# Performance work log

Hardware: AMD Instinct MI355X
Metric: run time of the kernel (lower is better)

## Reference

```python
import jax, jax.numpy as jnp
import numpy as np

N = 50000
E = 500000
H = 128


def _linear(x, w, b):
    # torch nn.Linear: y = x @ W.T + b, W is [out, in]
    return x @ w.T + b


def _layer(x, h, edge_index, w0_w, w0_b, wl_w, wl_b, w1_w, w1_b):
    # PyG MessagePassing(aggr='add', flow='target_to_source'):
    # x_j = h[edge_index[1]], scatter-add into edge_index[0], dim_size = N
    msg = h[edge_index[1]]                               # [E, H] gather
    aggr = jax.ops.segment_sum(msg, edge_index[0], num_segments=h.shape[0])  # [N, H]
    return _linear(aggr, wl_w, wl_b) + _linear(h, w0_w, w0_b) + _linear(x, w1_w, w1_b)


def setup_inputs() -> dict:
    key = jax.random.key(0)
    ks = jax.random.split(key, 12)
    wscale = 0.05
    return {
        "x_a": jax.random.normal(ks[0], (N, H), jnp.float32),
        "x_b": jax.random.normal(ks[1], (N, H), jnp.float32),
        "edge_ab": jax.random.randint(ks[2], (2, E), 0, N, jnp.int32),
        "edge_ba": jax.random.randint(ks[3], (2, E), 0, N, jnp.int32),
        "conv0_w0_w": jax.random.normal(ks[4], (H, H), jnp.float32) * wscale,
        "conv0_w0_b": jnp.zeros((H,), jnp.float32),
        "conv0_wl_w": jax.random.normal(ks[5], (H, H), jnp.float32) * wscale,
        "conv0_wl_b": jnp.zeros((H,), jnp.float32),
        "conv0_w1_w": jax.random.normal(ks[6], (H, H), jnp.float32) * wscale,
        "conv0_w1_b": jnp.zeros((H,), jnp.float32),
        "conv1_w0_w": jax.random.normal(ks[7], (H, H), jnp.float32) * wscale,
        "conv1_w0_b": jnp.zeros((H,), jnp.float32),
        "conv1_wl_w": jax.random.normal(ks[8], (H, H), jnp.float32) * wscale,
        "conv1_wl_b": jnp.zeros((H,), jnp.float32),
        "conv1_w1_w": jax.random.normal(ks[9], (H, H), jnp.float32) * wscale,
        "conv1_w1_b": jnp.zeros((H,), jnp.float32),
        "out_w": jax.random.normal(ks[10], (H, H), jnp.float32) * wscale,
        "out_b": jnp.zeros((H,), jnp.float32),
    }


def reference(x_a, x_b, edge_ab, edge_ba,
              conv0_w0_w, conv0_w0_b, conv0_wl_w, conv0_wl_b, conv0_w1_w, conv0_w1_b,
              conv1_w0_w, conv1_w0_b, conv1_wl_w, conv1_wl_b, conv1_w1_w, conv1_w1_b,
              out_w, out_b):
    # metapath = [(a, r1, b), (b, r2, a)], loop over reversed(metapath):
    # iter 0: conv_idx=1, edge (b, r2, a), dst='a'
    h_a = jax.nn.relu(_layer(x_a, x_a, edge_ba,
                             conv1_w0_w, conv1_w0_b, conv1_wl_w, conv1_wl_b, conv1_w1_w, conv1_w1_b))
    # iter 1: conv_idx=0, edge (a, r1, b), dst='b'
    h_b = jax.nn.relu(_layer(x_b, x_b, edge_ab,
                             conv0_w0_w, conv0_w0_b, conv0_wl_w, conv0_wl_b, conv0_w1_w, conv0_w1_b))
    # start_type = 'a'
    return _linear(h_a, out_w, out_b)
```

## Files before the change

kernel.cpp:

```cpp
#include <hip/hip_runtime.h>
#include <hip/hip_bf16.h>

#define NN 50000
#define NE 500000
#define HD 128
#define CAP 128
#define PREP_B 24
#define ZCUR_B ((NN + 255) / 256)
#define ZAGGR_B 6250
#define FILLB_B ((NE + 255) / 256)
#define XCONV_B 3125
#define K2_B (FILLB_B + XCONV_B)

typedef __bf16 bf16;
typedef __attribute__((ext_vector_type(8))) __bf16 bf16x8;
typedef __attribute__((ext_vector_type(4))) float floatx4;

__device__ inline float u2f(unsigned int lo16) {
    union { unsigned int i; float f; } c; c.i = lo16 << 16; return c.f;
}

__device__ inline bf16x8 cvt8(floatx4 a, floatx4 b) {
    bf16x8 r;
#pragma unroll
    for (int j = 0; j < 4; j++) { r[j] = (bf16)a[j]; r[j + 4] = (bf16)b[j]; }
    return r;
}

__device__ inline void split8(const floatx4 f0, const floatx4 f1, bf16x8& hi, bf16x8& lo) {
#pragma unroll
    for (int j = 0; j < 4; j++) {
        float a = f0[j]; bf16 h = (bf16)a; hi[j] = h; lo[j] = (bf16)(a - (float)h);
        float b = f1[j]; bf16 g = (bf16)b; hi[j + 4] = g; lo[j + 4] = (bf16)(b - (float)g);
    }
}

__device__ inline bf16x8 zero8() {
    bf16x8 v;
#pragma unroll
    for (int j = 0; j < 8; j++) v[j] = (bf16)0.f;
    return v;
}

__device__ inline void addrow(floatx4& f0, floatx4& f1, const uint4 v) {
    f0[0] += u2f(v.x & 0xffff); f0[1] += u2f(v.x >> 16);
    f0[2] += u2f(v.y & 0xffff); f0[3] += u2f(v.y >> 16);
    f1[0] += u2f(v.z & 0xffff); f1[1] += u2f(v.z >> 16);
    f1[2] += u2f(v.w & 0xffff); f1[3] += u2f(v.w >> 16);
}

__global__ __launch_bounds__(256) void k_setup1(
    const float* __restrict__ wl, const float* __restrict__ w0, const float* __restrict__ w1,
    const float* __restrict__ bl, const float* __restrict__ b0, const float* __restrict__ b1,
    const float* __restrict__ ow, const float* __restrict__ ob,
    bf16* __restrict__ wlb, bf16* __restrict__ w01b, bf16* __restrict__ owb,
    float* __restrict__ bias1, float* __restrict__ bias2,
    float* __restrict__ aggr, int* __restrict__ cur, int* __restrict__ ovf_cnt, int tier)
{
    const int b = blockIdx.x, tid = threadIdx.x;
    if (b < PREP_B) {
        int g = b * 256 + tid;
        int m = g >> 11, off = (g & 2047) << 3;
        if (m == 0) {
            const floatx4 a = *(const floatx4*)(wl + off);
            const floatx4 c = *(const floatx4*)(wl + off + 4);
            *(bf16x8*)(wlb + off) = cvt8(a, c);
        } else if (m == 1) {
            floatx4 a = *(const floatx4*)(w0 + off);
            floatx4 c = *(const floatx4*)(w0 + off + 4);
            const floatx4 d = *(const floatx4*)(w1 + off);
            const floatx4 e = *(const floatx4*)(w1 + off + 4);
#pragma unroll
            for (int j = 0; j < 4; j++) { a[j] += d[j]; c[j] += e[j]; }
            *(bf16x8*)(w01b + off) = cvt8(a, c);
        } else {
            const floatx4 a = *(const floatx4*)(ow + off);
            const floatx4 c = *(const floatx4*)(ow + off + 4);
            *(bf16x8*)(owb + off) = cvt8(a, c);
        }
        if (g < 128) bias1[g] = bl[g] + b0[g] + b1[g];
        else if (g < 256) bias2[g - 128] = ob[g - 128];
    } else if (b < PREP_B + ZCUR_B) {
        if (tier >= 1) {
            int i = (b - PREP_B) * 256 + tid;
            if (i < NN) cur[i] = 0;
            if (b == PREP_B && tid == 0) *ovf_cnt = 0;
        }
    } else {
        int i = (b - PREP_B - ZCUR_B) * 256 + tid;
        floatx4 z = {0.f, 0.f, 0.f, 0.f};
        ((floatx4*)aggr)[i] = z;
    }
}

__global__ __launch_bounds__(256) void k_setup2(
    const int* __restrict__ edge, const float* __restrict__ x,
    int* __restrict__ cur, int* __restrict__ bucket,
    int* __restrict__ ovf_cnt, int* __restrict__ ovf,
    bf16* __restrict__ xb)
{
    const int b = blockIdx.x, tid = threadIdx.x;
    if (b < FILLB_B) {
        int e = b * 256 + tid;
        if (e >= NE) return;
        int dst = edge[e];
        int src = edge[NE + e];
        int pos = atomicAdd(&cur[dst], 1);
        if (pos < CAP) {
            bucket[dst * CAP + pos] = src;
        } else {
            int oi = atomicAdd(ovf_cnt, 1);
            ovf[2 * oi] = dst;
            ovf[2 * oi + 1] = src;
        }
    } else {
        int off = ((b - FILLB_B) * 256 + tid) << 3;
        const floatx4 a = *(const floatx4*)(x + off);
        const floatx4 c = *(const floatx4*)(x + off + 4);
        *(bf16x8*)(xb + off) = cvt8(a, c);
    }
}

__global__ __launch_bounds__(256) void k_scatter(const float* __restrict__ x,
                                                 const int* __restrict__ edge,
                                                 float* __restrict__ aggr) {
    int tid = blockIdx.x * 256 + threadIdx.x;
    int e = tid >> 5;
    int c = (tid & 31) << 2;
    int dst = edge[e];
    int src = edge[NE + e];
    const floatx4 v = *(const floatx4*)(x + src * HD + c);
    float* ap = aggr + dst * HD + c;
    unsafeAtomicAdd(ap + 0, v[0]);
    unsafeAtomicAdd(ap + 1, v[1]);
    unsafeAtomicAdd(ap + 2, v[2]);
    unsafeAtomicAdd(ap + 3, v[3]);
}

__global__ __launch_bounds__(256) void k_fused(
    const float* __restrict__ aggr, const float* __restrict__ x, const bf16* __restrict__ xb,
    int tier,
    const int* __restrict__ cur, const int* __restrict__ bucket,
    const int* __restrict__ ovf_cnt, const int* __restrict__ ovf,
    const bf16* __restrict__ wlb, const bf16* __restrict__ w01b, const bf16* __restrict__ owb,
    const float* __restrict__ bias1, const float* __restrict__ bias2,
    float* __restrict__ out)
{
    __shared__ bf16 sA[128 * 136];
    __shared__ bf16 sB[128 * 136];
    __shared__ float b1_s[128], b2_s[128];
    float* tp = (float*)sB;
    const int tid = threadIdx.x;

#pragma unroll
    for (int it = 0; it < 8; it++) {
        int i = tid + it * 256;
        int r = i >> 4;
        int o = (i & 15) << 3;
        *(bf16x8*)(sA + r * 136 + o) = *(const bf16x8*)(wlb  + r * 128 + o);
        *(bf16x8*)(sB + r * 136 + o) = *(const bf16x8*)(w01b + r * 128 + o);
    }
    if (tid < 128) { b1_s[tid] = bias1[tid]; b2_s[tid] = bias2[tid]; }

    const int lane = tid & 63;
    const int wv   = tid >> 6;
    const int ln   = lane & 15;
    const int quad = lane >> 4;
    const int row0 = blockIdx.x * 64 + wv * 16;
    const int arow = row0 + ln;
    const bool aok = arow < NN;
    const int q8   = quad * 8;

    floatx4 ag0[4] = {};
    floatx4 ag1[4] = {};

    if (tier) {
        int deg = 0, n = 0;
        if (aok) { deg = cur[arow]; n = (deg < CAP) ? deg : CAP; }
        const int* bk = bucket + (size_t)arow * CAP;
        int t = 0;
        for (; t + 1 < n; t += 2) {
            const int s0 = bk[t], s1 = bk[t + 1];
            const bf16* r0 = xb + (size_t)s0 * HD + q8;
            const bf16* r1 = xb + (size_t)s1 * HD + q8;
            const uint4 a0 = *(const uint4*)(r0);
            const uint4 a1 = *(const uint4*)(r0 + 32);
            const uint4 a2 = *(const uint4*)(r0 + 64);
            const uint4 a3 = *(const uint4*)(r0 + 96);
            const uint4 c0 = *(const uint4*)(r1);
            const uint4 c1 = *(const uint4*)(r1 + 32);
            const uint4 c2 = *(const uint4*)(r1 + 64);
            const uint4 c3 = *(const uint4*)(r1 + 96);
            addrow(ag0[0], ag1[0], a0); addrow(ag0[1], ag1[1], a1);
            addrow(ag0[2], ag1[2], a2); addrow(ag0[3], ag1[3], a3);
            addrow(ag0[0], ag1[0], c0); addrow(ag0[1], ag1[1], c1);
            addrow(ag0[2], ag1[2], c2); addrow(ag0[3], ag1[3], c3);
        }
        if (t < n) {
            const int s0 = bk[t];
            const bf16* r0 = xb + (size_t)s0 * HD + q8;
            const uint4 a0 = *(const uint4*)(r0);
            const uint4 a1 = *(const uint4*)(r0 + 32);
            const uint4 a2 = *(const uint4*)(r0 + 64);
            const uint4 a3 = *(const uint4*)(r0 + 96);
            addrow(ag0[0], ag1[0], a0); addrow(ag0[1], ag1[1], a1);
            addrow(ag0[2], ag1[2], a2); addrow(ag0[3], ag1[3], a3);
        }
        if (deg > CAP) {
            const int m = *ovf_cnt;
            for (int i = 0; i < m; i++) {
                if (ovf[2 * i] == arow) {
                    const bf16* r0 = xb + (size_t)ovf[2 * i + 1] * HD + q8;
                    const uint4 a0 = *(const uint4*)(r0);
                    const uint4 a1 = *(const uint4*)(r0 + 32);
                    const uint4 a2 = *(const uint4*)(r0 + 64);
                    const uint4 a3 = *(const uint4*)(r0 + 96);
                    addrow(ag0[0], ag1[0], a0); addrow(ag0[1], ag1[1], a1);
                    addrow(ag0[2], ag1[2], a2); addrow(ag0[3], ag1[3], a3);
                }
            }
        }
    } else if (aok) {
#pragma unroll
        for (int kc = 0; kc < 4; kc++) {
            ag0[kc] = *(const floatx4*)(aggr + (size_t)arow * HD + kc * 32 + q8);
            ag1[kc] = *(const floatx4*)(aggr + (size_t)arow * HD + kc * 32 + q8 + 4);
        }
    }

    __syncthreads();

    floatx4 acc[8] = {};

#pragma unroll
    for (int kc = 0; kc < 4; kc++) {
        const int k0 = kc * 32 + q8;
        bf16x8 a_hi, a_lo;
        split8(ag0[kc], ag1[kc], a_hi, a_lo);
        bf16x8 a_x = zero8();
        if (aok) {
            if (tier) {
                a_x = *(const bf16x8*)(xb + (size_t)arow * HD + k0);
            } else {
                const floatx4 g0 = *(const floatx4*)(x + (size_t)arow * HD + k0);
                const floatx4 g1 = *(const floatx4*)(x + (size_t)arow * HD + k0 + 4);
                a_x = cvt8(g0, g1);
            }
        }
#pragma unroll
        for (int nc = 0; nc < 8; nc++) {
            const bf16x8 bw  = *(const bf16x8*)(sA + (nc * 16 + ln) * 136 + k0);
            const bf16x8 bw2 = *(const bf16x8*)(sB + (nc * 16 + ln) * 136 + k0);
            acc[nc] = __builtin_amdgcn_mfma_f32_16x16x32_bf16(a_hi, bw,  acc[nc], 0, 0, 0);
            acc[nc] = __builtin_amdgcn_mfma_f32_16x16x32_bf16(a_lo, bw,  acc[nc], 0, 0, 0);
            acc[nc] = __builtin_amdgcn_mfma_f32_16x16x32_bf16(a_x,  bw2, acc[nc], 0, 0, 0);
        }
    }
    __syncthreads();

#pragma unroll
    for (int it = 0; it < 8; it++) {
        int i = tid + it * 256;
        int r = i >> 4;
        int o = (i & 15) << 3;
        *(bf16x8*)(sA + r * 136 + o) = *(const bf16x8*)(owb + r * 128 + o);
    }
#pragma unroll
    for (int nc = 0; nc < 8; nc++) {
        const int col = nc * 16 + ln;
        const float bv = b1_s[col];
#pragma unroll
        for (int r = 0; r < 4; r++) {
            float v = acc[nc][r] + bv;
            tp[wv * 2112 + (quad * 4 + r) * 132 + col] = (v > 0.f ? v : 0.f);
        }
        acc[nc][0] = acc[nc][1] = acc[nc][2] = acc[nc][3] = 0.f;
    }
    __syncthreads();

#pragma unroll
    for (int kc = 0; kc < 4; kc++) {
        const int k0 = kc * 32 + q8;
        const floatx4 f0 = *(const floatx4*)(tp + wv * 2112 + ln * 132 + k0);
        const floatx4 f1 = *(const floatx4*)(tp + wv * 2112 + ln * 132 + k0 + 4);
        bf16x8 a_hi, a_lo;
        split8(f0, f1, a_hi, a_lo);
#pragma unroll
        for (int nc = 0; nc < 8; nc++) {
            const bf16x8 bw = *(const bf16x8*)(sA + (nc * 16 + ln) * 136 + k0);
            acc[nc] = __builtin_amdgcn_mfma_f32_16x16x32_bf16(a_hi, bw, acc[nc], 0, 0, 0);
            acc[nc] = __builtin_amdgcn_mfma_f32_16x16x32_bf16(a_lo, bw, acc[nc], 0, 0, 0);
        }
    }

#pragma unroll
    for (int nc = 0; nc < 8; nc++) {
        const int col = nc * 16 + ln;
        const float bv = b2_s[col];
#pragma unroll
        for (int r = 0; r < 4; r++) {
            const int row = row0 + quad * 4 + r;
            if (row < NN) out[row * 128 + col] = acc[nc][r] + bv;
        }
    }
}

extern "C" void kernel_launch(void* const* d_in, const int* in_sizes, int n_in,
                              void* d_out, int out_size, void* d_ws, size_t ws_size,
                              hipStream_t stream) {
    const float* x_a     = (const float*)d_in[0];
    const int*   edge_ba = (const int*)d_in[3];
    const float* c1_w0_w = (const float*)d_in[10];
    const float* c1_w0_b = (const float*)d_in[11];
    const float* c1_wl_w = (const float*)d_in[12];
    const float* c1_wl_b = (const float*)d_in[13];
    const float* c1_w1_w = (const float*)d_in[14];
    const float* c1_w1_b = (const float*)d_in[15];
    const float* out_w   = (const float*)d_in[16];
    const float* out_b   = (const float*)d_in[17];

    char* p = (char*)d_ws;
    float* aggr  = (float*)p;   p += (size_t)NN * HD * 4;
    bf16*  wlb   = (bf16*)p;    p += 32768;
    bf16*  w01b  = (bf16*)p;    p += 32768;
    bf16*  owb   = (bf16*)p;    p += 32768;
    float* bias1 = (float*)p;   p += 512;
    float* bias2 = (float*)p;   p += 512;
    const size_t WS_FALL = (size_t)(p - (char*)d_ws);
    int*   cur    = (int*)p;    p += 200704;
    int*   bucket = (int*)p;    p += (size_t)NN * CAP * 4;
    bf16*  xb     = (bf16*)p;   p += (size_t)NN * HD * 2;
    int*   ovf_cnt= (int*)p;    p += 256;
    int*   ovf    = (int*)p;    p += (size_t)NE * 2 * 4;
    const size_t WS_BUCKET = (size_t)(p - (char*)d_ws);
    (void)WS_FALL;

    const int tier = (ws_size >= WS_BUCKET) ? 1 : 0;

    const int k1_grid = tier ? (PREP_B + ZCUR_B) : (PREP_B + ZCUR_B + ZAGGR_B);
    k_setup1<<<k1_grid, 256, 0, stream>>>(c1_wl_w, c1_w0_w, c1_w1_w,
                                          c1_wl_b, c1_w0_b, c1_w1_b,
                                          out_w, out_b,
                                          wlb, w01b, owb, bias1, bias2,
                                          aggr, cur, ovf_cnt, tier);

    if (tier) {
        k_setup2<<<K2_B, 256, 0, stream>>>(edge_ba, x_a, cur, bucket, ovf_cnt, ovf, xb);
    } else {
        k_scatter<<<NE * 32 / 256, 256, 0, stream>>>(x_a, edge_ba, aggr);
    }

    k_fused<<<(NN + 63) / 64, 256, 0, stream>>>(aggr, x_a, xb, tier,
                                                cur, bucket, ovf_cnt, ovf,
                                                wlb, w01b, owb, bias1, bias2,
                                                (float*)d_out);
}
```

Before: 192.9 us.

## Read weights directly from global memory, drop LDS staging and block barriers

Removes the shared-memory staging of the three bf16 weight matrices and biases, so the MFMA B operands are read straight from global memory (expected to hit cache). Shared memory shrinks to a per-wave scratch tile for the hidden activations, which removes all __syncthreads and adds a launch-bounds hint of 4 blocks per CU to raise occupancy. Also loads bucket indices two at a time as an int2. In exchange, every wave issues its own global or L2 loads for the weights instead of sharing one LDS copy, which adds memory traffic and latency to the MFMA loop.

```diff
diff --git a/kernel.cpp b/kernel.cpp
--- a/kernel.cpp
+++ b/kernel.cpp
@@ -137,7 +137,7 @@
     unsafeAtomicAdd(ap + 3, v[3]);
 }
 
-__global__ __launch_bounds__(256) void k_fused(
+__global__ __launch_bounds__(256, 4) void k_fused(
     const float* __restrict__ aggr, const float* __restrict__ x, const bf16* __restrict__ xb,
     int tier,
     const int* __restrict__ cur, const int* __restrict__ bucket,
@@ -146,22 +146,8 @@
     const float* __restrict__ bias1, const float* __restrict__ bias2,
     float* __restrict__ out)
 {
-    __shared__ bf16 sA[128 * 136];
-    __shared__ bf16 sB[128 * 136];
-    __shared__ float b1_s[128], b2_s[128];
-    float* tp = (float*)sB;
-    const int tid = threadIdx.x;
-
-#pragma unroll
-    for (int it = 0; it < 8; it++) {
-        int i = tid + it * 256;
-        int r = i >> 4;
-        int o = (i & 15) << 3;
-        *(bf16x8*)(sA + r * 136 + o) = *(const bf16x8*)(wlb  + r * 128 + o);
-        *(bf16x8*)(sB + r * 136 + o) = *(const bf16x8*)(w01b + r * 128 + o);
-    }
-    if (tid < 128) { b1_s[tid] = bias1[tid]; b2_s[tid] = bias2[tid]; }
-
+    __shared__ float tp[4 * 16 * 132];
+    const int tid  = threadIdx.x;
     const int lane = tid & 63;
     const int wv   = tid >> 6;
     const int ln   = lane & 15;
@@ -170,6 +156,7 @@
     const int arow = row0 + ln;
     const bool aok = arow < NN;
     const int q8   = quad * 8;
+    float* mytp = tp + wv * 2112;
 
     floatx4 ag0[4] = {};
     floatx4 ag1[4] = {};
@@ -180,9 +167,9 @@
         const int* bk = bucket + (size_t)arow * CAP;
         int t = 0;
         for (; t + 1 < n; t += 2) {
-            const int s0 = bk[t], s1 = bk[t + 1];
-            const bf16* r0 = xb + (size_t)s0 * HD + q8;
-            const bf16* r1 = xb + (size_t)s1 * HD + q8;
+            const int2 s = *(const int2*)(bk + t);
+            const bf16* r0 = xb + (size_t)s.x * HD + q8;
+            const bf16* r1 = xb + (size_t)s.y * HD + q8;
             const uint4 a0 = *(const uint4*)(r0);
             const uint4 a1 = *(const uint4*)(r0 + 32);
             const uint4 a2 = *(const uint4*)(r0 + 64);
@@ -228,8 +215,6 @@
         }
     }
 
-    __syncthreads();
-
     floatx4 acc[8] = {};
 
 #pragma unroll
@@ -249,45 +234,36 @@
         }
 #pragma unroll
         for (int nc = 0; nc < 8; nc++) {
-            const bf16x8 bw  = *(const bf16x8*)(sA + (nc * 16 + ln) * 136 + k0);
-            const bf16x8 bw2 = *(const bf16x8*)(sB + (nc * 16 + ln) * 136 + k0);
+            const bf16x8 bw  = *(const bf16x8*)(wlb  + (nc * 16 + ln) * HD + k0);
+            const bf16x8 bw2 = *(const bf16x8*)(w01b + (nc * 16 + ln) * HD + k0);
             acc[nc] = __builtin_amdgcn_mfma_f32_16x16x32_bf16(a_hi, bw,  acc[nc], 0, 0, 0);
             acc[nc] = __builtin_amdgcn_mfma_f32_16x16x32_bf16(a_lo, bw,  acc[nc], 0, 0, 0);
             acc[nc] = __builtin_amdgcn_mfma_f32_16x16x32_bf16(a_x,  bw2, acc[nc], 0, 0, 0);
         }
     }
-    __syncthreads();
-
-#pragma unroll
-    for (int it = 0; it < 8; it++) {
-        int i = tid + it * 256;
-        int r = i >> 4;
-        int o = (i & 15) << 3;
-        *(bf16x8*)(sA + r * 136 + o) = *(const bf16x8*)(owb + r * 128 + o);
-    }
+
 #pragma unroll
     for (int nc = 0; nc < 8; nc++) {
         const int col = nc * 16 + ln;
-        const float bv = b1_s[col];
+        const float bv = bias1[col];
 #pragma unroll
         for (int r = 0; r < 4; r++) {
             float v = acc[nc][r] + bv;
-            tp[wv * 2112 + (quad * 4 + r) * 132 + col] = (v > 0.f ? v : 0.f);
+            mytp[(quad * 4 + r) * 132 + col] = (v > 0.f ? v : 0.f);
         }
         acc[nc][0] = acc[nc][1] = acc[nc][2] = acc[nc][3] = 0.f;
     }
-    __syncthreads();
 
 #pragma unroll
     for (int kc = 0; kc < 4; kc++) {
         const int k0 = kc * 32 + q8;
-        const floatx4 f0 = *(const floatx4*)(tp + wv * 2112 + ln * 132 + k0);
-        const floatx4 f1 = *(const floatx4*)(tp + wv * 2112 + ln * 132 + k0 + 4);
+        const floatx4 f0 = *(const floatx4*)(mytp + ln * 132 + k0);
+        const floatx4 f1 = *(const floatx4*)(mytp + ln * 132 + k0 + 4);
         bf16x8 a_hi, a_lo;
         split8(f0, f1, a_hi, a_lo);
 #pragma unroll
         for (int nc = 0; nc < 8; nc++) {
-            const bf16x8 bw = *(const bf16x8*)(sA + (nc * 16 + ln) * 136 + k0);
+            const bf16x8 bw = *(const bf16x8*)(owb + (nc * 16 + ln) * HD + k0);
             acc[nc] = __builtin_amdgcn_mfma_f32_16x16x32_bf16(a_hi, bw, acc[nc], 0, 0, 0);
             acc[nc] = __builtin_amdgcn_mfma_f32_16x16x32_bf16(a_lo, bw, acc[nc], 0, 0, 0);
         }
@@ -296,7 +272,7 @@
 #pragma unroll
     for (int nc = 0; nc < 8; nc++) {
         const int col = nc * 16 + ln;
-        const float bv = b2_s[col];
+        const float bv = bias2[col];
 #pragma unroll
         for (int r = 0; r < 4; r++) {
             const int row = row0 + quad * 4 + r;
```

New measurement: 223.3 us. 15.8% more time.

## Software-pipeline neighbor gathers four at a time with double-buffered registers

Applied to the files above, without the earlier changes.

Replaces the two-at-a-time neighbor gather loop with a loop that loads four bucket indices as one int4 and issues sixteen 16-byte row loads per step. Two register sets alternate so the next group's loads are in flight while the previous group is unpacked and accumulated. The node's own bf16 row is now loaded before the gather instead of inside the MFMA loop. Launch bounds request two blocks per SM. The larger register footprint may cause spills or lower occupancy, and the added nullptr check on bias2 is effectively a no-op.

```diff
diff --git a/kernel.cpp b/kernel.cpp
--- a/kernel.cpp
+++ b/kernel.cpp
@@ -48,6 +48,28 @@
     f1[0] += u2f(v.z & 0xffff); f1[1] += u2f(v.z >> 16);
     f1[2] += u2f(v.w & 0xffff); f1[3] += u2f(v.w >> 16);
 }
+
+#define GLOAD16(v, S) do { \
+    const uint4* p0_ = (const uint4*)(xb + (size_t)(S).x * HD + q8); \
+    const uint4* p1_ = (const uint4*)(xb + (size_t)(S).y * HD + q8); \
+    const uint4* p2_ = (const uint4*)(xb + (size_t)(S).z * HD + q8); \
+    const uint4* p3_ = (const uint4*)(xb + (size_t)(S).w * HD + q8); \
+    v##00 = p0_[0]; v##01 = p0_[4]; v##02 = p0_[8]; v##03 = p0_[12]; \
+    v##10 = p1_[0]; v##11 = p1_[4]; v##12 = p1_[8]; v##13 = p1_[12]; \
+    v##20 = p2_[0]; v##21 = p2_[4]; v##22 = p2_[8]; v##23 = p2_[12]; \
+    v##30 = p3_[0]; v##31 = p3_[4]; v##32 = p3_[8]; v##33 = p3_[12]; \
+} while (0)
+
+#define GUNPACK(v) do { \
+    addrow(ag0[0], ag1[0], v##00); addrow(ag0[1], ag1[1], v##01); \
+    addrow(ag0[2], ag1[2], v##02); addrow(ag0[3], ag1[3], v##03); \
+    addrow(ag0[0], ag1[0], v##10); addrow(ag0[1], ag1[1], v##11); \
+    addrow(ag0[2], ag1[2], v##12); addrow(ag0[3], ag1[3], v##13); \
+    addrow(ag0[0], ag1[0], v##20); addrow(ag0[1], ag1[1], v##21); \
+    addrow(ag0[2], ag1[2], v##22); addrow(ag0[3], ag1[3], v##23); \
+    addrow(ag0[0], ag1[0], v##30); addrow(ag0[1], ag1[1], v##31); \
+    addrow(ag0[2], ag1[2], v##32); addrow(ag0[3], ag1[3], v##33); \
+} while (0)
 
 __global__ __launch_bounds__(256) void k_setup1(
     const float* __restrict__ wl, const float* __restrict__ w0, const float* __restrict__ w1,
@@ -137,7 +159,7 @@
     unsafeAtomicAdd(ap + 3, v[3]);
 }
 
-__global__ __launch_bounds__(256) void k_fused(
+__global__ __launch_bounds__(256, 2) void k_fused(
     const float* __restrict__ aggr, const float* __restrict__ x, const bf16* __restrict__ xb,
     int tier,
     const int* __restrict__ cur, const int* __restrict__ bucket,
@@ -174,49 +196,64 @@
     floatx4 ag0[4] = {};
     floatx4 ag1[4] = {};
 
+    bf16x8 ax[4] = {zero8(), zero8(), zero8(), zero8()};
+    if (tier && aok) {
+#pragma unroll
+        for (int kc = 0; kc < 4; kc++)
+            ax[kc] = *(const bf16x8*)(xb + (size_t)arow * HD + kc * 32 + q8);
+    }
+
     if (tier) {
         int deg = 0, n = 0;
         if (aok) { deg = cur[arow]; n = (deg < CAP) ? deg : CAP; }
         const int* bk = bucket + (size_t)arow * CAP;
         int t = 0;
-        for (; t + 1 < n; t += 2) {
-            const int s0 = bk[t], s1 = bk[t + 1];
-            const bf16* r0 = xb + (size_t)s0 * HD + q8;
-            const bf16* r1 = xb + (size_t)s1 * HD + q8;
-            const uint4 a0 = *(const uint4*)(r0);
-            const uint4 a1 = *(const uint4*)(r0 + 32);
-            const uint4 a2 = *(const uint4*)(r0 + 64);
-            const uint4 a3 = *(const uint4*)(r0 + 96);
-            const uint4 c0 = *(const uint4*)(r1);
-            const uint4 c1 = *(const uint4*)(r1 + 32);
-            const uint4 c2 = *(const uint4*)(r1 + 64);
-            const uint4 c3 = *(const uint4*)(r1 + 96);
-            addrow(ag0[0], ag1[0], a0); addrow(ag0[1], ag1[1], a1);
-            addrow(ag0[2], ag1[2], a2); addrow(ag0[3], ag1[3], a3);
-            addrow(ag0[0], ag1[0], c0); addrow(ag0[1], ag1[1], c1);
-            addrow(ag0[2], ag1[2], c2); addrow(ag0[3], ag1[3], c3);
-        }
-        if (t < n) {
-            const int s0 = bk[t];
-            const bf16* r0 = xb + (size_t)s0 * HD + q8;
-            const uint4 a0 = *(const uint4*)(r0);
-            const uint4 a1 = *(const uint4*)(r0 + 32);
-            const uint4 a2 = *(const uint4*)(r0 + 64);
-            const uint4 a3 = *(const uint4*)(r0 + 96);
-            addrow(ag0[0], ag1[0], a0); addrow(ag0[1], ag1[1], a1);
-            addrow(ag0[2], ag1[2], a2); addrow(ag0[3], ag1[3], a3);
+        uint4 a00, a01, a02, a03, a10, a11, a12, a13,
+              a20, a21, a22, a23, a30, a31, a32, a33;
+        uint4 b00, b01, b02, b03, b10, b11, b12, b13,
+              b20, b21, b22, b23, b30, b31, b32, b33;
+        if (t + 3 < n) {
+            int4 si = *(const int4*)(bk);
+            GLOAD16(a, si);
+            t = 4;
+            while (t + 3 < n) {
+                const int4 sj = *(const int4*)(bk + t);
+                GLOAD16(b, sj);
+                t += 4;
+                GUNPACK(a);
+                if (t + 3 < n) {
+                    si = *(const int4*)(bk + t);
+                    GLOAD16(a, si);
+                    t += 4;
+                    GUNPACK(b);
+                } else {
+                    GUNPACK(b);
+                    goto gdone;
+                }
+            }
+            GUNPACK(a);
+gdone:      ;
+        }
+        for (; t < n; t++) {
+            const bf16* r0 = xb + (size_t)bk[t] * HD + q8;
+            const uint4 e0 = *(const uint4*)(r0);
+            const uint4 e1 = *(const uint4*)(r0 + 32);
+            const uint4 e2 = *(const uint4*)(r0 + 64);
+            const uint4 e3 = *(const uint4*)(r0 + 96);
+            addrow(ag0[0], ag1[0], e0); addrow(ag0[1], ag1[1], e1);
+            addrow(ag0[2], ag1[2], e2); addrow(ag0[3], ag1[3], e3);
         }
         if (deg > CAP) {
             const int m = *ovf_cnt;
             for (int i = 0; i < m; i++) {
                 if (ovf[2 * i] == arow) {
                     const bf16* r0 = xb + (size_t)ovf[2 * i + 1] * HD + q8;
-                    const uint4 a0 = *(const uint4*)(r0);
-                    const uint4 a1 = *(const uint4*)(r0 + 32);
-                    const uint4 a2 = *(const uint4*)(r0 + 64);
-                    const uint4 a3 = *(const uint4*)(r0 + 96);
-                    addrow(ag0[0], ag1[0], a0); addrow(ag0[1], ag1[1], a1);
-                    addrow(ag0[2], ag1[2], a2); addrow(ag0[3], ag1[3], a3);
+                    const uint4 e0 = *(const uint4*)(r0);
+                    const uint4 e1 = *(const uint4*)(r0 + 32);
+                    const uint4 e2 = *(const uint4*)(r0 + 64);
+                    const uint4 e3 = *(const uint4*)(r0 + 96);
+                    addrow(ag0[0], ag1[0], e0); addrow(ag0[1], ag1[1], e1);
+                    addrow(ag0[2], ag1[2], e2); addrow(ag0[3], ag1[3], e3);
                 }
             }
         }
@@ -237,15 +274,11 @@
         const int k0 = kc * 32 + q8;
         bf16x8 a_hi, a_lo;
         split8(ag0[kc], ag1[kc], a_hi, a_lo);
-        bf16x8 a_x = zero8();
-        if (aok) {
-            if (tier) {
-                a_x = *(const bf16x8*)(xb + (size_t)arow * HD + k0);
-            } else {
-                const floatx4 g0 = *(const floatx4*)(x + (size_t)arow * HD + k0);
-                const floatx4 g1 = *(const floatx4*)(x + (size_t)arow * HD + k0 + 4);
-                a_x = cvt8(g0, g1);
-            }
+        bf16x8 a_x = ax[kc];
+        if (!tier && aok) {
+            const floatx4 g0 = *(const floatx4*)(x + (size_t)arow * HD + k0);
+            const floatx4 g1 = *(const floatx4*)(x + (size_t)arow * HD + k0 + 4);
+            a_x = cvt8(g0, g1);
         }
 #pragma unroll
         for (int nc = 0; nc < 8; nc++) {
@@ -296,7 +329,7 @@
 #pragma unroll
     for (int nc = 0; nc < 8; nc++) {
         const int col = nc * 16 + ln;
-        const float bv = b2_s[col];
+        const float bv = bias2 == nullptr ? 0.f : b2_s[col];
 #pragma unroll
         for (int r = 0; r < 4; r++) {
             const int row = row0 + quad * 4 + r;
```

After: 260.3 us. +34.9%, slower.
